# Kernel optimization log

Measured on AMD Instinct MI355X. Metric: run time of the kernel, lower is better.

The kernel has to match this reference:

```python
import jax, jax.numpy as jnp
import numpy as np

B, S, D, H = 8, 2048, 512, 2
DK = D  # per-head dim (d_k=d_v=in_dim in source)
OUT = 512
EPS = 1e-5


def setup_inputs() -> dict:
    key = jax.random.key(0)
    ks = jax.random.split(key, 20)
    sc = lambda fan_in: 1.0 / np.sqrt(fan_in)
    inp = {
        "x": jax.random.normal(ks[0], (B, S, D), jnp.float32),
        "skip": jax.random.normal(ks[1], (B, S, D), jnp.float32),
        # attention projections: d_model -> h*d_k
        "Wq": jax.random.normal(ks[2], (H * DK, D), jnp.float32) * sc(D),
        "bq": jnp.zeros((H * DK,), jnp.float32),
        "Wk": jax.random.normal(ks[3], (H * DK, D), jnp.float32) * sc(D),
        "bk": jnp.zeros((H * DK,), jnp.float32),
        "Wv": jax.random.normal(ks[4], (H * DK, D), jnp.float32) * sc(D),
        "bv": jnp.zeros((H * DK,), jnp.float32),
        "Wo": jax.random.normal(ks[5], (D, H * DK), jnp.float32) * sc(H * DK),
        "bo": jnp.zeros((D,), jnp.float32),
        # post linear in_dim -> out_dim
        "Wl": jax.random.normal(ks[6], (OUT, D), jnp.float32) * sc(D),
        "bl": jnp.zeros((OUT,), jnp.float32),
        # LayerNorm params
        "gamma": jnp.ones((OUT,), jnp.float32),
        "beta": jnp.zeros((OUT,), jnp.float32),
        # proj(skip): Linear(512 -> out_dim)
        "Wp": jax.random.normal(ks[7], (OUT, D), jnp.float32) * sc(D),
        "bp": jnp.zeros((OUT,), jnp.float32),
    }
    return inp


def _upblock(x, skip, Wq, bq, Wk, bk, Wv, bv, Wo, bo, Wl, bl, gamma, beta, Wp, bp):
    # multi-head scaled dot-product self-attention (hand-rolled, as in source)
    q = (x @ Wq.T + bq).reshape(B, S, H, DK)  # bshd
    k = (x @ Wk.T + bk).reshape(B, S, H, DK)
    v = (x @ Wv.T + bv).reshape(B, S, H, DK)
    scores = jnp.einsum("bqhd,bkhd->bhqk", q, k) / jnp.sqrt(jnp.float32(DK))
    att = jax.nn.softmax(scores, axis=-1)
    o = jnp.einsum("bhqk,bkhd->bqhd", att, v).reshape(B, S, H * DK)
    o = o @ Wo.T + bo  # [B,S,D]
    # SiLU -> Linear -> LayerNorm
    h = jax.nn.silu(o) @ Wl.T + bl  # [B,S,OUT]
    mu = jnp.mean(h, axis=-1, keepdims=True)
    var = jnp.mean(jnp.square(h - mu), axis=-1, keepdims=True)
    h = (h - mu) * jax.lax.rsqrt(var + EPS) * gamma + beta
    # residual with projected skip
    return h + (skip @ Wp.T + bp)


def reference(x, skip, Wq, bq, Wk, bk, Wv, bv, Wo, bo, Wl, bl, gamma, beta, Wp, bp):
    return _upblock(x, skip, Wq, bq, Wk, bk, Wv, bv, Wo, bo, Wl, bl, gamma, beta, Wp, bp)
```

## Files before the change

### kernel.cpp

```cpp
#include <hip/hip_runtime.h>
#include <math.h>

typedef unsigned short u16;
typedef u16 u16x8 __attribute__((ext_vector_type(8)));
typedef __bf16 bf16x8 __attribute__((ext_vector_type(8)));
typedef float f32x4 __attribute__((ext_vector_type(4)));

#define MBL (1LL << 20)

__device__ __forceinline__ u16 f2bf(float x) {
    unsigned u = __float_as_uint(x);
    return (u16)((u + 0x7fffu + ((u >> 16) & 1u)) >> 16);
}
__device__ __forceinline__ float bf2f(u16 h) { return __uint_as_float(((unsigned)h) << 16); }
__device__ __forceinline__ float silu_f(float x) { return x / (1.f + __expf(-x)); }

#define GLDS(gp, off) __builtin_amdgcn_global_load_lds( \
    (const __attribute__((address_space(1))) void*)(gp), \
    (__attribute__((address_space(3))) void*)(&SL[off]), 16, 0, 0)

template<int SPLITA, int EPI>
__global__ __launch_bounds__(256)
void gemm_ss(const float* __restrict__ Af,
             const u16* __restrict__ Ah, const u16* __restrict__ Al,
             const u16* __restrict__ Bh, const u16* __restrict__ Bl,
             float* __restrict__ Cf, u16* __restrict__ Ch, u16* __restrict__ Cl,
             float* __restrict__ rsum,
             long lda, long ldb, long ldc, int K, float alpha,
             const float* __restrict__ bias,
             const float* __restrict__ addp, long ldadd,
             long sAb, long sAh2, long sBb, long sBh2, long sCb, long sCh2)
{
    const int z = blockIdx.z, zb = z >> 1, zh = z & 1;
    const long offA = (long)zb * sAb + (long)zh * sAh2;
    const long offB = (long)zb * sBb + (long)zh * sBh2;
    const long offC = (long)zb * sCb + (long)zh * sCh2;
    if (SPLITA) { Ah += offA; Al += offA; } else { Af += offA; }
    Bh += offB; Bl += offB;
    if (EPI == 0) Cf += offC; else { Ch += offC; Cl += offC; }
    if (EPI >= 3) rsum += (long)z * 2048;

    __shared__ u16 SL[16384];
    const int AH = 0, AL = 4096, BH = 8192, BL = 12288;

    const int tid = threadIdx.x;
    const int wave = tid >> 6, lane = tid & 63;
    const long m0 = (long)blockIdx.y * 128;
    const long n0 = (long)blockIdx.x * 128;

    const int lrow = lane >> 2;
    const int kcol = (lane & 3) << 3;
    const int ldsW = wave * 512;

    const int srow = tid >> 1;
    const int sh   = (tid & 1) << 4;
    const float* gA = SPLITA ? nullptr : (Af + (m0 + srow) * lda + sh);
    const int sB = srow * 32 + sh;

    const int wr = (wave >> 1) << 6;
    const int wc = (wave & 1) << 6;
    const int fr = lane & 15;
    const int fk = (lane >> 4) << 3;

    f32x4 acc[4][4];
#pragma unroll
    for (int i = 0; i < 4; ++i)
#pragma unroll
        for (int j = 0; j < 4; ++j) acc[i][j] = (f32x4)0.f;

    for (int kb = 0; kb < K; kb += 32) {
        float a[16];
        if (!SPLITA) {
            *(float4*)&a[0]  = *(const float4*)(gA + kb);
            *(float4*)&a[4]  = *(const float4*)(gA + kb + 4);
            *(float4*)&a[8]  = *(const float4*)(gA + kb + 8);
            *(float4*)&a[12] = *(const float4*)(gA + kb + 12);
        }
        __syncthreads();
#pragma unroll
        for (int t = 0; t < 2; ++t) {
            const long row = wave * 16 + lrow + t * 64;
            GLDS(Bh + (n0 + row) * ldb + kb + kcol, BH + ldsW + t * 2048);
            GLDS(Bl + (n0 + row) * ldb + kb + kcol, BL + ldsW + t * 2048);
            if (SPLITA) {
                GLDS(Ah + (m0 + row) * lda + kb + kcol, AH + ldsW + t * 2048);
                GLDS(Al + (m0 + row) * lda + kb + kcol, AL + ldsW + t * 2048);
            }
        }
        if (!SPLITA) {
            u16 hv[16], lv[16];
#pragma unroll
            for (int u = 0; u < 16; ++u) {
                u16 h = f2bf(a[u]); hv[u] = h; lv[u] = f2bf(a[u] - bf2f(h));
            }
            *(u16x8*)&SL[AH + sB]     = *(u16x8*)&hv[0];
            *(u16x8*)&SL[AH + sB + 8] = *(u16x8*)&hv[8];
            *(u16x8*)&SL[AL + sB]     = *(u16x8*)&lv[0];
            *(u16x8*)&SL[AL + sB + 8] = *(u16x8*)&lv[8];
        }
        __syncthreads();

        bf16x8 fah[4], fal[4], fbh[4], fbl[4];
#pragma unroll
        for (int i = 0; i < 4; ++i) {
            const int r = (wr + (i << 4) + fr) * 32 + fk;
            fah[i] = *(const bf16x8*)&SL[AH + r];
            fal[i] = *(const bf16x8*)&SL[AL + r];
        }
#pragma unroll
        for (int j = 0; j < 4; ++j) {
            const int r = (wc + (j << 4) + fr) * 32 + fk;
            fbh[j] = *(const bf16x8*)&SL[BH + r];
            fbl[j] = *(const bf16x8*)&SL[BL + r];
        }
#pragma unroll
        for (int i = 0; i < 4; ++i)
#pragma unroll
            for (int j = 0; j < 4; ++j) {
                acc[i][j] = __builtin_amdgcn_mfma_f32_16x16x32_bf16(fah[i], fbh[j], acc[i][j], 0, 0, 0);
                acc[i][j] = __builtin_amdgcn_mfma_f32_16x16x32_bf16(fah[i], fbl[j], acc[i][j], 0, 0, 0);
                acc[i][j] = __builtin_amdgcn_mfma_f32_16x16x32_bf16(fal[i], fbh[j], acc[i][j], 0, 0, 0);
            }
    }

    const int rl = (lane >> 4) << 2;
#pragma unroll
    for (int i = 0; i < 4; ++i) {
#pragma unroll
        for (int r2 = 0; r2 < 4; ++r2) {
            const long row = m0 + wr + (i << 4) + rl + r2;
            float psum = 0.f;
            float rinv = 0.f;
            if (EPI == 4) rinv = 1.f / rsum[row];
#pragma unroll
            for (int j = 0; j < 4; ++j) {
                const long col = n0 + wc + (j << 4) + fr;
                float c = acc[i][j][r2];
                if (EPI == 0 || EPI == 1 || EPI == 2) {
                    c = c * alpha + (bias ? bias[col] : 0.f);
                }
                if (EPI == 0) {
                    if (addp) c += addp[row * ldadd + col];
                    Cf[row * ldc + col] = c;
                } else if (EPI == 1 || EPI == 2) {
                    if (EPI == 2) c = silu_f(c);
                    u16 h = f2bf(c);
                    Ch[row * ldc + col] = h;
                    Cl[row * ldc + col] = f2bf(c - bf2f(h));
                } else if (EPI == 3) {
                    float p = __expf(c * alpha);
                    psum += p;
                    u16 h = f2bf(p);
                    Ch[row * ldc + col] = h;
                    Cl[row * ldc + col] = f2bf(p - bf2f(h));
                } else {
                    c *= rinv;
                    u16 h = f2bf(c);
                    Ch[row * ldc + col] = h;
                    Cl[row * ldc + col] = f2bf(c - bf2f(h));
                }
            }
            if (EPI == 3) {
                psum += __shfl_xor(psum, 1);
                psum += __shfl_xor(psum, 2);
                psum += __shfl_xor(psum, 4);
                psum += __shfl_xor(psum, 8);
                if ((lane & 15) == 0) atomicAdd(&rsum[row], psum);
            }
        }
    }
}

__global__ __launch_bounds__(256)
void split_f32(const float* __restrict__ in, u16* __restrict__ hi, u16* __restrict__ lo)
{
    const long i = (((long)blockIdx.x << 8) + threadIdx.x) << 3;
    float4 v0 = *(const float4*)(in + i), v1 = *(const float4*)(in + i + 4);
    float f[8] = {v0.x, v0.y, v0.z, v0.w, v1.x, v1.y, v1.z, v1.w};
    u16x8 h8, l8;
#pragma unroll
    for (int u = 0; u < 8; ++u) { u16 h = f2bf(f[u]); h8[u] = h; l8[u] = f2bf(f[u] - bf2f(h)); }
    *(u16x8*)(hi + i) = h8;
    *(u16x8*)(lo + i) = l8;
}

__global__ __launch_bounds__(256)
void transpose_vs(const float* __restrict__ v, u16* __restrict__ vth, u16* __restrict__ vtl,
                  long sVb, long sVh, long sTb, long sTh)
{
    const int z = blockIdx.z, s = z >> 1, h = z & 1;
    const float* src = v + (long)s * sVb + (long)h * sVh;
    u16* dh = vth + (long)s * sTb + (long)h * sTh;
    u16* dl = vtl + (long)s * sTb + (long)h * sTh;
    __shared__ float T[64][68];
    const int t = threadIdx.x;
    const int r = t >> 2, c0 = (t & 3) << 4;
    const long sBase = (long)blockIdx.x * 64;
    const long dBase = (long)blockIdx.y * 64;
    const float* sp = src + (sBase + r) * 1024 + dBase + c0;
#pragma unroll
    for (int q = 0; q < 4; ++q)
        *(float4*)&T[r][c0 + 4 * q] = *(const float4*)(sp + 4 * q);
    __syncthreads();
    u16x8 h8[2], l8[2];
#pragma unroll
    for (int g = 0; g < 2; ++g)
#pragma unroll
        for (int u = 0; u < 8; ++u) {
            float f = T[c0 + g * 8 + u][r];
            u16 h = f2bf(f);
            h8[g][u] = h; l8[g][u] = f2bf(f - bf2f(h));
        }
    const long o = (dBase + r) * 2048 + sBase + c0;
    *(u16x8*)&dh[o] = h8[0]; *(u16x8*)&dh[o + 8] = h8[1];
    *(u16x8*)&dl[o] = l8[0]; *(u16x8*)&dl[o + 8] = l8[1];
}

__global__ __launch_bounds__(256)
void layernorm_rows(const float* __restrict__ h,
                    const float* __restrict__ gamma,
                    const float* __restrict__ beta,
                    float* __restrict__ o)
{
    const int lane = threadIdx.x & 63;
    const long row = ((long)blockIdx.x << 2) + (threadIdx.x >> 6);
    const float* hr = h + row * 512;
    float v[8];
    *(float4*)&v[0] = *(const float4*)(hr + (lane << 3));
    *(float4*)&v[4] = *(const float4*)(hr + (lane << 3) + 4);
    float s = 0.f;
#pragma unroll
    for (int i = 0; i < 8; ++i) s += v[i];
#pragma unroll
    for (int off = 32; off >= 1; off >>= 1) s += __shfl_xor(s, off);
    const float mu = s * (1.f / 512.f);
    float sq = 0.f;
#pragma unroll
    for (int i = 0; i < 8; ++i) { v[i] -= mu; sq = fmaf(v[i], v[i], sq); }
#pragma unroll
    for (int off = 32; off >= 1; off >>= 1) sq += __shfl_xor(sq, off);
    const float rs = rsqrtf(sq * (1.f / 512.f) + 1e-5f);
    float g[8], b[8];
    *(float4*)&g[0] = *(const float4*)(gamma + (lane << 3));
    *(float4*)&g[4] = *(const float4*)(gamma + (lane << 3) + 4);
    *(float4*)&b[0] = *(const float4*)(beta + (lane << 3));
    *(float4*)&b[4] = *(const float4*)(beta + (lane << 3) + 4);
    float ov[8];
#pragma unroll
    for (int i = 0; i < 8; ++i) ov[i] = fmaf(v[i] * rs, g[i], b[i]);
    float* orow = o + row * 512;
    *(float4*)(orow + (lane << 3))     = *(float4*)&ov[0];
    *(float4*)(orow + (lane << 3) + 4) = *(float4*)&ov[4];
}

extern "C" void kernel_launch(void* const* d_in, const int* in_sizes, int n_in,
                              void* d_out, int out_size, void* d_ws, size_t ws_size,
                              hipStream_t stream)
{
    const float* x    = (const float*)d_in[0];
    const float* skip = (const float*)d_in[1];
    const float* Wq   = (const float*)d_in[2];
    const float* bq   = (const float*)d_in[3];
    const float* Wk   = (const float*)d_in[4];
    const float* bk   = (const float*)d_in[5];
    const float* Wv   = (const float*)d_in[6];
    const float* bv   = (const float*)d_in[7];
    const float* Wo   = (const float*)d_in[8];
    const float* bo   = (const float*)d_in[9];
    const float* Wl   = (const float*)d_in[10];
    const float* bl   = (const float*)d_in[11];
    const float* gm   = (const float*)d_in[12];
    const float* bt   = (const float*)d_in[13];
    const float* Wp   = (const float*)d_in[14];
    const float* bp   = (const float*)d_in[15];
    float* out = (float*)d_out;

    char* W = (char*)d_ws;
    u16* wqh = (u16*)(W);
    u16* wql = wqh + 524288;
    u16* wkh = wql + 524288;  u16* wkl = wkh + 524288;
    u16* wvh = wkl + 524288;  u16* wvl = wvh + 524288;
    u16* woh = wvl + 524288;  u16* wol = woh + 524288;
    u16* wlh = wol + 524288;  u16* wll = wlh + 262144;
    u16* wph = wll + 262144;  u16* wpl = wph + 262144;
    float* rsum = (float*)(W + 10 * MBL);
    u16* ahi  = (u16*)(W + 16 * MBL);
    u16* alo  = (u16*)(W + 48 * MBL);
    u16* ophi = (u16*)(W + 80 * MBL);
    u16* oplo = (u16*)(W + 96 * MBL);
    float* hb  = (float*)(W + 16 * MBL);
    float* lnh = (float*)(W + 48 * MBL);
    char* PB = W + 112 * MBL;

    long avail = (long)ws_size - 112 * MBL;
    long gbl = avail / (56 * MBL);
    int gb = gbl < 1 ? 1 : (gbl > 8 ? 8 : (int)gbl);

    const long SLOT_U = 29360128;
    const long SLOT_F = 14680064;
    u16*   qh0 = (u16*)(PB);
    u16*   kh0 = (u16*)(PB + 8 * MBL);
    u16*   vth0 = (u16*)(PB + 16 * MBL);
    u16*   ph0 = (u16*)(PB + 24 * MBL);
    float* vtm0 = (float*)(PB + 24 * MBL);

    const float sscale = 0.044194173824159216f;
    const long Z = 0;

    hipMemsetAsync(rsum, 0, 16 * 2048 * 4, stream);

    split_f32<<<256, 256, 0, stream>>>(Wq, wqh, wql);
    split_f32<<<256, 256, 0, stream>>>(Wk, wkh, wkl);
    split_f32<<<256, 256, 0, stream>>>(Wv, wvh, wvl);
    split_f32<<<256, 256, 0, stream>>>(Wo, woh, wol);
    split_f32<<<128, 256, 0, stream>>>(Wl, wlh, wll);
    split_f32<<<128, 256, 0, stream>>>(Wp, wph, wpl);

    for (int b0 = 0; b0 < 8; b0 += gb) {
        const int gc = (8 - b0) < gb ? (8 - b0) : gb;
        const float* xg = x + (long)b0 * 1048576;
        gemm_ss<0, 1><<<dim3(8, 16, gc), 256, 0, stream>>>(
            xg, nullptr, nullptr, wqh, wql, nullptr, qh0, qh0 + 2097152, nullptr,
            512, 512, 1024, 512, 1.f, bq, nullptr, 0,
            2097152L, 1048576L, Z, Z, 2 * SLOT_U, SLOT_U);
        gemm_ss<0, 1><<<dim3(8, 16, gc), 256, 0, stream>>>(
            xg, nullptr, nullptr, wkh, wkl, nullptr, kh0, kh0 + 2097152, nullptr,
            512, 512, 1024, 512, 1.f, bk, nullptr, 0,
            2097152L, 1048576L, Z, Z, 2 * SLOT_U, SLOT_U);
        gemm_ss<0, 0><<<dim3(8, 16, gc), 256, 0, stream>>>(
            xg, nullptr, nullptr, wvh, wvl, vtm0, nullptr, nullptr, nullptr,
            512, 512, 1024, 512, 1.f, bv, nullptr, 0,
            2097152L, 1048576L, Z, Z, 2 * SLOT_F, SLOT_F);
        transpose_vs<<<dim3(32, 8, 2 * gc), 256, 0, stream>>>(
            vtm0, vth0, vth0 + 1048576,
            SLOT_F, 512, SLOT_U, 2097152L);
        gemm_ss<1, 3><<<dim3(16, 16, 2 * gc), 256, 0, stream>>>(
            nullptr, qh0, qh0 + 2097152, kh0, kh0 + 2097152,
            nullptr, ph0, ph0 + 2048, rsum + (long)b0 * 4096,
            1024, 1024, 4096, 512, sscale, nullptr, nullptr, 0,
            SLOT_U, 512, SLOT_U, 512, SLOT_U, 8388608L);
        gemm_ss<1, 4><<<dim3(4, 16, 2 * gc), 256, 0, stream>>>(
            nullptr, ph0, ph0 + 2048, vth0, vth0 + 1048576,
            nullptr, ahi + (long)b0 * 2097152, alo + (long)b0 * 2097152,
            rsum + (long)b0 * 4096,
            4096, 2048, 1024, 2048, 1.f, nullptr, nullptr, 0,
            SLOT_U, 8388608L, SLOT_U, 2097152L, 2097152L, 512);
    }

    gemm_ss<1, 2><<<dim3(4, 128, 1), 256, 0, stream>>>(
        nullptr, ahi, alo, woh, wol, nullptr, ophi, oplo, nullptr,
        1024, 1024, 512, 1024, 1.f, bo, nullptr, 0, Z, Z, Z, Z, Z, Z);
    gemm_ss<1, 0><<<dim3(4, 128, 1), 256, 0, stream>>>(
        nullptr, ophi, oplo, wlh, wll, hb, nullptr, nullptr, nullptr,
        512, 512, 512, 512, 1.f, bl, nullptr, 0, Z, Z, Z, Z, Z, Z);
    layernorm_rows<<<4096, 256, 0, stream>>>(hb, gm, bt, lnh);
    gemm_ss<0, 0><<<dim3(4, 128, 1), 256, 0, stream>>>(
        skip, nullptr, nullptr, wph, wpl, out, nullptr, nullptr, nullptr,
        512, 512, 512, 512, 1.f, bp, lnh, 512, Z, Z, Z, Z, Z, Z);
}
```

Measured before the change: 1.450 ms.

## Fuse QKV projections into one GEMM, swizzle LDS layout, transpose V from bf16

Concatenates Wq/Wk/Wv and their biases so one GEMM produces Q, K and V as split bf16 hi/lo with ld 3072, instead of three launches plus an fp32 V buffer. V is now transposed directly from the bf16 halves, with no fp32 read and no re-splitting. The LDS tile layout gets an XOR swizzle on the k-chunk index to reduce bank conflicts on the fragment reads. A per-head sequential fallback is added for small workspaces, which changes the workspace layout and the z-indexing parameters.

After: 1.304 ms. 1.11x faster.

```diff
diff --git a/kernel.cpp b/kernel.cpp
--- a/kernel.cpp
+++ b/kernel.cpp
@@ -29,16 +29,19 @@
              long lda, long ldb, long ldc, int K, float alpha,
              const float* __restrict__ bias,
              const float* __restrict__ addp, long ldadd,
+             int zshift, int hbase, long rstride,
              long sAb, long sAh2, long sBb, long sBh2, long sCb, long sCh2)
 {
-    const int z = blockIdx.z, zb = z >> 1, zh = z & 1;
+    const int z = blockIdx.z;
+    const int zb = z >> zshift;
+    const int zh = (z & ((1 << zshift) - 1)) + hbase;
     const long offA = (long)zb * sAb + (long)zh * sAh2;
     const long offB = (long)zb * sBb + (long)zh * sBh2;
     const long offC = (long)zb * sCb + (long)zh * sCh2;
     if (SPLITA) { Ah += offA; Al += offA; } else { Af += offA; }
     Bh += offB; Bl += offB;
     if (EPI == 0) Cf += offC; else { Ch += offC; Cl += offC; }
-    if (EPI >= 3) rsum += (long)z * 2048;
+    if (EPI >= 3) rsum += (long)z * rstride;
 
     __shared__ u16 SL[16384];
     const int AH = 0, AL = 4096, BH = 8192, BL = 12288;
@@ -48,19 +51,24 @@
     const long m0 = (long)blockIdx.y * 128;
     const long n0 = (long)blockIdx.x * 128;
 
-    const int lrow = lane >> 2;
-    const int kcol = (lane & 3) << 3;
-    const int ldsW = wave * 512;
+    const int prow = (wave << 4) + (lane >> 2);
+    const int k8s  = ((lane & 3) ^ ((prow >> 1) & 3)) << 3;
+    const long aoff0 = (m0 + prow) * lda + k8s;
+    const long aoff1 = (m0 + prow + 64) * lda + k8s;
+    const long boff0 = (n0 + prow) * ldb + k8s;
+    const long boff1 = (n0 + prow + 64) * ldb + k8s;
+    const int ldsW = wave << 9;
 
     const int srow = tid >> 1;
-    const int sh   = (tid & 1) << 4;
-    const float* gA = SPLITA ? nullptr : (Af + (m0 + srow) * lda + sh);
-    const int sB = srow * 32 + sh;
+    const float* gA = SPLITA ? nullptr : (Af + (m0 + srow) * lda + ((tid & 1) << 4));
+    const int fs   = (srow >> 1) & 3;
+    const int sA0  = srow * 32 + (((((tid & 1) << 1) + 0) ^ fs) << 3);
+    const int sA1  = srow * 32 + (((((tid & 1) << 1) + 1) ^ fs) << 3);
 
     const int wr = (wave >> 1) << 6;
     const int wc = (wave & 1) << 6;
     const int fr = lane & 15;
-    const int fk = (lane >> 4) << 3;
+    const int kph = (((lane >> 4) ^ ((fr >> 1) & 3)) << 3);
 
     f32x4 acc[4][4];
 #pragma unroll
@@ -77,39 +85,38 @@
             *(float4*)&a[12] = *(const float4*)(gA + kb + 12);
         }
         __syncthreads();
-#pragma unroll
-        for (int t = 0; t < 2; ++t) {
-            const long row = wave * 16 + lrow + t * 64;
-            GLDS(Bh + (n0 + row) * ldb + kb + kcol, BH + ldsW + t * 2048);
-            GLDS(Bl + (n0 + row) * ldb + kb + kcol, BL + ldsW + t * 2048);
-            if (SPLITA) {
-                GLDS(Ah + (m0 + row) * lda + kb + kcol, AH + ldsW + t * 2048);
-                GLDS(Al + (m0 + row) * lda + kb + kcol, AL + ldsW + t * 2048);
-            }
-        }
-        if (!SPLITA) {
+        GLDS(Bh + boff0 + kb, BH + ldsW);
+        GLDS(Bh + boff1 + kb, BH + ldsW + 2048);
+        GLDS(Bl + boff0 + kb, BL + ldsW);
+        GLDS(Bl + boff1 + kb, BL + ldsW + 2048);
+        if (SPLITA) {
+            GLDS(Ah + aoff0 + kb, AH + ldsW);
+            GLDS(Ah + aoff1 + kb, AH + ldsW + 2048);
+            GLDS(Al + aoff0 + kb, AL + ldsW);
+            GLDS(Al + aoff1 + kb, AL + ldsW + 2048);
+        } else {
             u16 hv[16], lv[16];
 #pragma unroll
             for (int u = 0; u < 16; ++u) {
                 u16 h = f2bf(a[u]); hv[u] = h; lv[u] = f2bf(a[u] - bf2f(h));
             }
-            *(u16x8*)&SL[AH + sB]     = *(u16x8*)&hv[0];
-            *(u16x8*)&SL[AH + sB + 8] = *(u16x8*)&hv[8];
-            *(u16x8*)&SL[AL + sB]     = *(u16x8*)&lv[0];
-            *(u16x8*)&SL[AL + sB + 8] = *(u16x8*)&lv[8];
+            *(u16x8*)&SL[AH + sA0] = *(u16x8*)&hv[0];
+            *(u16x8*)&SL[AH + sA1] = *(u16x8*)&hv[8];
+            *(u16x8*)&SL[AL + sA0] = *(u16x8*)&lv[0];
+            *(u16x8*)&SL[AL + sA1] = *(u16x8*)&lv[8];
         }
         __syncthreads();
 
         bf16x8 fah[4], fal[4], fbh[4], fbl[4];
 #pragma unroll
         for (int i = 0; i < 4; ++i) {
-            const int r = (wr + (i << 4) + fr) * 32 + fk;
+            const int r = (wr + (i << 4) + fr) * 32 + kph;
             fah[i] = *(const bf16x8*)&SL[AH + r];
             fal[i] = *(const bf16x8*)&SL[AL + r];
         }
 #pragma unroll
         for (int j = 0; j < 4; ++j) {
-            const int r = (wc + (j << 4) + fr) * 32 + fk;
+            const int r = (wc + (j << 4) + fr) * 32 + kph;
             fbh[j] = *(const bf16x8*)&SL[BH + r];
             fbl[j] = *(const bf16x8*)&SL[BL + r];
         }
@@ -185,35 +192,46 @@
 }
 
 __global__ __launch_bounds__(256)
-void transpose_vs(const float* __restrict__ v, u16* __restrict__ vth, u16* __restrict__ vtl,
+void concat_b(const float* __restrict__ a, const float* __restrict__ b,
+              const float* __restrict__ c, float* __restrict__ d)
+{
+    const int i = blockIdx.x * 256 + threadIdx.x;
+    d[i] = i < 1024 ? a[i] : (i < 2048 ? b[i - 1024] : c[i - 2048]);
+}
+
+__global__ __launch_bounds__(256)
+void transpose_vs(const u16* __restrict__ vh, const u16* __restrict__ vl,
+                  u16* __restrict__ th, u16* __restrict__ tl,
                   long sVb, long sVh, long sTb, long sTh)
 {
-    const int z = blockIdx.z, s = z >> 1, h = z & 1;
-    const float* src = v + (long)s * sVb + (long)h * sVh;
-    u16* dh = vth + (long)s * sTb + (long)h * sTh;
-    u16* dl = vtl + (long)s * sTb + (long)h * sTh;
-    __shared__ float T[64][68];
+    const int z = blockIdx.z, zb = z >> 1, zh = z & 1;
+    const u16* sh_ = vh + (long)zb * sVb + (long)zh * sVh;
+    const u16* sl_ = vl + (long)zb * sVb + (long)zh * sVh;
+    u16* dh = th + (long)zb * sTb + (long)zh * sTh;
+    u16* dl = tl + (long)zb * sTb + (long)zh * sTh;
+    __shared__ u16 Th[64][72], Tl[64][72];
     const int t = threadIdx.x;
-    const int r = t >> 2, c0 = (t & 3) << 4;
+    const int r0 = t >> 3;
+    const int c8 = (t & 7) << 3;
     const long sBase = (long)blockIdx.x * 64;
     const long dBase = (long)blockIdx.y * 64;
-    const float* sp = src + (sBase + r) * 1024 + dBase + c0;
-#pragma unroll
-    for (int q = 0; q < 4; ++q)
-        *(float4*)&T[r][c0 + 4 * q] = *(const float4*)(sp + 4 * q);
+#pragma unroll
+    for (int rr = 0; rr < 64; rr += 32) {
+        const long so = (sBase + r0 + rr) * 3072 + dBase + c8;
+        *(u16x8*)&Th[r0 + rr][c8] = *(const u16x8*)(sh_ + so);
+        *(u16x8*)&Tl[r0 + rr][c8] = *(const u16x8*)(sl_ + so);
+    }
     __syncthreads();
-    u16x8 h8[2], l8[2];
-#pragma unroll
-    for (int g = 0; g < 2; ++g)
-#pragma unroll
-        for (int u = 0; u < 8; ++u) {
-            float f = T[c0 + g * 8 + u][r];
-            u16 h = f2bf(f);
-            h8[g][u] = h; l8[g][u] = f2bf(f - bf2f(h));
-        }
-    const long o = (dBase + r) * 2048 + sBase + c0;
-    *(u16x8*)&dh[o] = h8[0]; *(u16x8*)&dh[o + 8] = h8[1];
-    *(u16x8*)&dl[o] = l8[0]; *(u16x8*)&dl[o + 8] = l8[1];
+#pragma unroll
+    for (int rr = 0; rr < 64; rr += 32) {
+        const int dr = r0 + rr;
+        u16x8 oh, ol;
+#pragma unroll
+        for (int u = 0; u < 8; ++u) { oh[u] = Th[c8 + u][dr]; ol[u] = Tl[c8 + u][dr]; }
+        const long dofs = (dBase + dr) * 2048 + sBase + c8;
+        *(u16x8*)&dh[dofs] = oh;
+        *(u16x8*)&dl[dofs] = ol;
+    }
 }
 
 __global__ __launch_bounds__(256)
@@ -276,85 +294,108 @@
     float* out = (float*)d_out;
 
     char* W = (char*)d_ws;
-    u16* wqh = (u16*)(W);
-    u16* wql = wqh + 524288;
-    u16* wkh = wql + 524288;  u16* wkl = wkh + 524288;
-    u16* wvh = wkl + 524288;  u16* wvl = wvh + 524288;
-    u16* woh = wvl + 524288;  u16* wol = woh + 524288;
-    u16* wlh = wol + 524288;  u16* wll = wlh + 262144;
-    u16* wph = wll + 262144;  u16* wpl = wph + 262144;
-    float* rsum = (float*)(W + 10 * MBL);
-    u16* ahi  = (u16*)(W + 16 * MBL);
-    u16* alo  = (u16*)(W + 48 * MBL);
-    u16* ophi = (u16*)(W + 80 * MBL);
-    u16* oplo = (u16*)(W + 96 * MBL);
-    float* hb  = (float*)(W + 16 * MBL);
-    float* lnh = (float*)(W + 48 * MBL);
-    char* PB = W + 112 * MBL;
-
-    long avail = (long)ws_size - 112 * MBL;
-    long gbl = avail / (56 * MBL);
-    int gb = gbl < 1 ? 1 : (gbl > 8 ? 8 : (int)gbl);
-
-    const long SLOT_U = 29360128;
-    const long SLOT_F = 14680064;
-    u16*   qh0 = (u16*)(PB);
-    u16*   kh0 = (u16*)(PB + 8 * MBL);
-    u16*   vth0 = (u16*)(PB + 16 * MBL);
-    u16*   ph0 = (u16*)(PB + 24 * MBL);
-    float* vtm0 = (float*)(PB + 24 * MBL);
+    u16* wqkvh = (u16*)(W);
+    u16* wqkvl = (u16*)(W + 3 * MBL);
+    u16* woh   = (u16*)(W + 6 * MBL);
+    u16* wol   = (u16*)(W + 7 * MBL);
+    u16* wlh   = (u16*)(W + 8 * MBL);
+    u16* wll   = (u16*)(W + 8 * MBL + 512 * 1024);
+    u16* wph   = (u16*)(W + 9 * MBL);
+    u16* wpl   = (u16*)(W + 9 * MBL + 512 * 1024);
+    float* bqkv = (float*)(W + 10 * MBL);
+    float* rsum = (float*)(W + 10 * MBL + 65536);
+    u16* ahi  = (u16*)(W + 12 * MBL);
+    u16* alo  = (u16*)(W + 44 * MBL);
+    u16* ophi = (u16*)(W + 76 * MBL);
+    u16* oplo = (u16*)(W + 92 * MBL);
+    float* hb  = (float*)(W + 12 * MBL);
+    float* lnh = (float*)(W + 44 * MBL);
+    char* SLOTS = W + 108 * MBL;
+
+    long avail = (long)ws_size - 108 * MBL;
+    int gb; bool hseq;
+    if (avail >= 64 * MBL) {
+        hseq = false;
+        long g = avail / (64 * MBL);
+        gb = (int)(g > 8 ? 8 : g);
+    } else {
+        hseq = true; gb = 1;
+    }
+    const long SLOT_B = hseq ? 48 * MBL : 64 * MBL;
+    const long SLOT_U = SLOT_B >> 1;
+    u16* qkvh0 = (u16*)(SLOTS);
+    u16* qkvl0 = (u16*)(SLOTS + 12 * MBL);
+    u16* vth0  = (u16*)(SLOTS + 24 * MBL);
+    u16* ph0   = (u16*)(SLOTS + 32 * MBL);
 
     const float sscale = 0.044194173824159216f;
     const long Z = 0;
 
     hipMemsetAsync(rsum, 0, 16 * 2048 * 4, stream);
 
-    split_f32<<<256, 256, 0, stream>>>(Wq, wqh, wql);
-    split_f32<<<256, 256, 0, stream>>>(Wk, wkh, wkl);
-    split_f32<<<256, 256, 0, stream>>>(Wv, wvh, wvl);
+    split_f32<<<256, 256, 0, stream>>>(Wq, wqkvh, wqkvl);
+    split_f32<<<256, 256, 0, stream>>>(Wk, wqkvh + 524288, wqkvl + 524288);
+    split_f32<<<256, 256, 0, stream>>>(Wv, wqkvh + 1048576, wqkvl + 1048576);
     split_f32<<<256, 256, 0, stream>>>(Wo, woh, wol);
     split_f32<<<128, 256, 0, stream>>>(Wl, wlh, wll);
     split_f32<<<128, 256, 0, stream>>>(Wp, wph, wpl);
+    concat_b<<<12, 256, 0, stream>>>(bq, bk, bv, bqkv);
 
     for (int b0 = 0; b0 < 8; b0 += gb) {
         const int gc = (8 - b0) < gb ? (8 - b0) : gb;
-        const float* xg = x + (long)b0 * 1048576;
-        gemm_ss<0, 1><<<dim3(8, 16, gc), 256, 0, stream>>>(
-            xg, nullptr, nullptr, wqh, wql, nullptr, qh0, qh0 + 2097152, nullptr,
-            512, 512, 1024, 512, 1.f, bq, nullptr, 0,
-            2097152L, 1048576L, Z, Z, 2 * SLOT_U, SLOT_U);
-        gemm_ss<0, 1><<<dim3(8, 16, gc), 256, 0, stream>>>(
-            xg, nullptr, nullptr, wkh, wkl, nullptr, kh0, kh0 + 2097152, nullptr,
-            512, 512, 1024, 512, 1.f, bk, nullptr, 0,
-            2097152L, 1048576L, Z, Z, 2 * SLOT_U, SLOT_U);
-        gemm_ss<0, 0><<<dim3(8, 16, gc), 256, 0, stream>>>(
-            xg, nullptr, nullptr, wvh, wvl, vtm0, nullptr, nullptr, nullptr,
-            512, 512, 1024, 512, 1.f, bv, nullptr, 0,
-            2097152L, 1048576L, Z, Z, 2 * SLOT_F, SLOT_F);
+        gemm_ss<0, 1><<<dim3(24, 16, gc), 256, 0, stream>>>(
+            x + (long)b0 * 1048576, nullptr, nullptr, wqkvh, wqkvl,
+            nullptr, qkvh0, qkvl0, nullptr,
+            512, 512, 3072, 512, 1.f, bqkv, nullptr, 0,
+            0, 0, 0,
+            1048576L, Z, Z, Z, SLOT_U, Z);
         transpose_vs<<<dim3(32, 8, 2 * gc), 256, 0, stream>>>(
-            vtm0, vth0, vth0 + 1048576,
-            SLOT_F, 512, SLOT_U, 2097152L);
-        gemm_ss<1, 3><<<dim3(16, 16, 2 * gc), 256, 0, stream>>>(
-            nullptr, qh0, qh0 + 2097152, kh0, kh0 + 2097152,
-            nullptr, ph0, ph0 + 2048, rsum + (long)b0 * 4096,
-            1024, 1024, 4096, 512, sscale, nullptr, nullptr, 0,
-            SLOT_U, 512, SLOT_U, 512, SLOT_U, 8388608L);
-        gemm_ss<1, 4><<<dim3(4, 16, 2 * gc), 256, 0, stream>>>(
-            nullptr, ph0, ph0 + 2048, vth0, vth0 + 1048576,
-            nullptr, ahi + (long)b0 * 2097152, alo + (long)b0 * 2097152,
-            rsum + (long)b0 * 4096,
-            4096, 2048, 1024, 2048, 1.f, nullptr, nullptr, 0,
-            SLOT_U, 8388608L, SLOT_U, 2097152L, 2097152L, 512);
+            qkvh0 + 2048, qkvl0 + 2048, vth0, vth0 + 1048576,
+            SLOT_U, 512, SLOT_U, 2097152L);
+        if (!hseq) {
+            gemm_ss<1, 3><<<dim3(16, 16, 2 * gc), 256, 0, stream>>>(
+                nullptr, qkvh0, qkvl0, qkvh0 + 1024, qkvl0 + 1024,
+                nullptr, ph0, ph0 + 2048, rsum + (long)b0 * 4096,
+                3072, 3072, 4096, 512, sscale, nullptr, nullptr, 0,
+                1, 0, 2048,
+                SLOT_U, 512, SLOT_U, 512, SLOT_U, 8388608L);
+            gemm_ss<1, 4><<<dim3(4, 16, 2 * gc), 256, 0, stream>>>(
+                nullptr, ph0, ph0 + 2048, vth0, vth0 + 1048576,
+                nullptr, ahi + (long)b0 * 2097152, alo + (long)b0 * 2097152,
+                rsum + (long)b0 * 4096,
+                4096, 2048, 1024, 2048, 1.f, nullptr, nullptr, 0,
+                1, 0, 2048,
+                SLOT_U, 8388608L, SLOT_U, 2097152L, 2097152L, 512);
+        } else {
+            for (int h = 0; h < 2; ++h) {
+                gemm_ss<1, 3><<<dim3(16, 16, gc), 256, 0, stream>>>(
+                    nullptr, qkvh0, qkvl0, qkvh0 + 1024, qkvl0 + 1024,
+                    nullptr, ph0, ph0 + 2048, rsum + ((long)b0 * 2 + h) * 2048,
+                    3072, 3072, 4096, 512, sscale, nullptr, nullptr, 0,
+                    0, h, 4096,
+                    SLOT_U, 512, SLOT_U, 512, SLOT_U, Z);
+                gemm_ss<1, 4><<<dim3(4, 16, gc), 256, 0, stream>>>(
+                    nullptr, ph0, ph0 + 2048, vth0, vth0 + 1048576,
+                    nullptr, ahi + (long)b0 * 2097152, alo + (long)b0 * 2097152,
+                    rsum + ((long)b0 * 2 + h) * 2048,
+                    4096, 2048, 1024, 2048, 1.f, nullptr, nullptr, 0,
+                    0, h, 4096,
+                    SLOT_U, Z, SLOT_U, 2097152L, 2097152L, 512);
+            }
+        }
     }
 
     gemm_ss<1, 2><<<dim3(4, 128, 1), 256, 0, stream>>>(
         nullptr, ahi, alo, woh, wol, nullptr, ophi, oplo, nullptr,
-        1024, 1024, 512, 1024, 1.f, bo, nullptr, 0, Z, Z, Z, Z, Z, Z);
+        1024, 1024, 512, 1024, 1.f, bo, nullptr, 0,
+        0, 0, 0, Z, Z, Z, Z, Z, Z);
     gemm_ss<1, 0><<<dim3(4, 128, 1), 256, 0, stream>>>(
         nullptr, ophi, oplo, wlh, wll, hb, nullptr, nullptr, nullptr,
-        512, 512, 512, 512, 1.f, bl, nullptr, 0, Z, Z, Z, Z, Z, Z);
+        512, 512, 512, 512, 1.f, bl, nullptr, 0,
+        0, 0, 0, Z, Z, Z, Z, Z, Z);
     layernorm_rows<<<4096, 256, 0, stream>>>(hb, gm, bt, lnh);
     gemm_ss<0, 0><<<dim3(4, 128, 1), 256, 0, stream>>>(
         skip, nullptr, nullptr, wph, wpl, out, nullptr, nullptr, nullptr,
-        512, 512, 512, 512, 1.f, bp, lnh, 512, Z, Z, Z, Z, Z, Z);
-}
+        512, 512, 512, 512, 1.f, bp, lnh, 512,
+        0, 0, 0, Z, Z, Z, Z, Z, Z);
+}
```
